# Kernel optimization log

Hardware: AMD Instinct MI355X
Metric: run time of the kernel (lower is better)

The kernel has to match this reference:

```python
import jax, jax.numpy as jnp
import numpy as np

STRIDE = 1

def setup_inputs() -> dict:
    key = jax.random.key(0)
    k1, k2 = jax.random.split(key)
    x = jax.random.normal(k1, (64, 16384), dtype=jnp.float32)        # (B, L)
    kernel = jax.random.normal(k2, (128, 16), dtype=jnp.float32) * 0.05  # (F, K) == phi
    return {"x": x, "kernel": kernel}

def reference(x, kernel):
    # Faithful math of SpecCnn1d_v01.call: the sparse phi places kernel[f, j]
    # at (f, i, i*stride + j), so phi @ x^T == windowed dot product.
    B, L = x.shape
    F, K = kernel.shape
    out_len = (L - K) // STRIDE + 1  # floor((L + 2*0 - K)/stride) + 1
    # Sliding windows: (out_len, K) gather indices -> windows (B, out_len, K)
    idx = jnp.arange(out_len)[:, None] * STRIDE + jnp.arange(K)[None, :]
    windows = x[:, idx]                       # (B, O, K)
    y = jnp.einsum('bok,fk->bof', windows, kernel)  # (B, O, F), matches perm [2,1,0]
    return jax.nn.relu(y)                     # activation='relu', use_bias=False
```

## Files before the change

### kernel.cpp

```cpp
#include <hip/hip_runtime.h>


constexpr int K_TAPS  = 16;
constexpr int F_FILT  = 128;
constexpr int O_TILE  = 64;
constexpr int O_CHUNK = 8;

__global__ __launch_bounds__(F_FILT) void SpecCnn1d_conv_kernel(
    const float* __restrict__ x,
    const float* __restrict__ w,
    float* __restrict__ y,
    int L, int out_len)
{
    const int f  = threadIdx.x;
    const int b  = blockIdx.y;
    const int o0 = blockIdx.x * O_TILE;

    float wr[K_TAPS];
    const float4* w4 = reinterpret_cast<const float4*>(w + f * K_TAPS);
    #pragma unroll
    for (int i = 0; i < K_TAPS / 4; ++i) {
        float4 v = w4[i];
        wr[4 * i + 0] = v.x;
        wr[4 * i + 1] = v.y;
        wr[4 * i + 2] = v.z;
        wr[4 * i + 3] = v.w;
    }

    const float* xb = x + (size_t)b * L;
    float*       yb = y + ((size_t)b * out_len + o0) * F_FILT + f;

    for (int oc = 0; oc < O_TILE; oc += O_CHUNK) {
        const int base = o0 + oc;

        float xs[O_CHUNK + K_TAPS - 1];
        #pragma unroll
        for (int j = 0; j < O_CHUNK + K_TAPS - 1; ++j) {
            int xi = base + j;
            xi = (xi < L) ? xi : (L - 1);
            xs[j] = xb[xi];
        }

        #pragma unroll
        for (int oo = 0; oo < O_CHUNK; ++oo) {
            float acc = 0.0f;
            #pragma unroll
            for (int k = 0; k < K_TAPS; ++k)
                acc = fmaf(xs[oo + k], wr[k], acc);
            const int o = base + oo;
            if (o < out_len)
                yb[(size_t)(oc + oo) * F_FILT] = fmaxf(acc, 0.0f);
        }
    }
}

extern "C" void kernel_launch(void* const* d_in, const int* in_sizes, int n_in,
                              void* d_out, int out_size, void* d_ws, size_t ws_size,
                              hipStream_t stream) {
    const float* x = (const float*)d_in[0];
    const float* w = (const float*)d_in[1];
    float*       y = (float*)d_out;

    const int B = 64;
    const int L = in_sizes[0] / B;
    const int out_len = L - K_TAPS + 1;

    dim3 grid((out_len + O_TILE - 1) / O_TILE, B);
    dim3 block(F_FILT);
    SpecCnn1d_conv_kernel<<<grid, block, 0, stream>>>(x, w, y, L, out_len);
}
```

Before: 543.2 us.

## Register-block four filters per thread with float4 loads and stores

```diff
diff --git a/kernel.cpp b/kernel.cpp
--- a/kernel.cpp
+++ b/kernel.cpp
@@ -4,52 +4,96 @@
 constexpr int K_TAPS  = 16;
 constexpr int F_FILT  = 128;
 constexpr int O_TILE  = 64;
-constexpr int O_CHUNK = 8;
+constexpr int O_PER_T = 8;
+constexpr int NTHREAD = 256;
 
-__global__ __launch_bounds__(F_FILT) void SpecCnn1d_conv_kernel(
+__global__ __launch_bounds__(NTHREAD) void SpecCnn1d_conv_kernel(
     const float* __restrict__ x,
     const float* __restrict__ w,
     float* __restrict__ y,
     int L, int out_len)
 {
-    const int f  = threadIdx.x;
+    const int f4 = threadIdx.x & 31;
+    const int g  = threadIdx.x >> 5;
     const int b  = blockIdx.y;
     const int o0 = blockIdx.x * O_TILE;
+    const int f  = f4 * 4;
 
-    float wr[K_TAPS];
-    const float4* w4 = reinterpret_cast<const float4*>(w + f * K_TAPS);
+    float wr[4][K_TAPS];
     #pragma unroll
-    for (int i = 0; i < K_TAPS / 4; ++i) {
-        float4 v = w4[i];
-        wr[4 * i + 0] = v.x;
-        wr[4 * i + 1] = v.y;
-        wr[4 * i + 2] = v.z;
-        wr[4 * i + 3] = v.w;
+    for (int ff = 0; ff < 4; ++ff) {
+        const float4* w4 = reinterpret_cast<const float4*>(w + (size_t)(f + ff) * K_TAPS);
+        #pragma unroll
+        for (int i = 0; i < K_TAPS / 4; ++i) {
+            float4 v = w4[i];
+            wr[ff][4 * i + 0] = v.x;
+            wr[ff][4 * i + 1] = v.y;
+            wr[ff][4 * i + 2] = v.z;
+            wr[ff][4 * i + 3] = v.w;
+        }
     }
 
     const float* xb = x + (size_t)b * L;
-    float*       yb = y + ((size_t)b * out_len + o0) * F_FILT + f;
+    const int    s  = o0 + g * O_PER_T;
+    float*       yb = y + ((size_t)b * out_len + s) * F_FILT + f;
 
-    for (int oc = 0; oc < O_TILE; oc += O_CHUNK) {
-        const int base = o0 + oc;
+    float xs[O_PER_T + K_TAPS];
 
-        float xs[O_CHUNK + K_TAPS - 1];
+    if (o0 + O_TILE + K_TAPS <= L) {
+        const float4* xv = reinterpret_cast<const float4*>(xb + s);
         #pragma unroll
-        for (int j = 0; j < O_CHUNK + K_TAPS - 1; ++j) {
-            int xi = base + j;
+        for (int i = 0; i < (O_PER_T + K_TAPS) / 4; ++i) {
+            float4 v = xv[i];
+            xs[4 * i + 0] = v.x;
+            xs[4 * i + 1] = v.y;
+            xs[4 * i + 2] = v.z;
+            xs[4 * i + 3] = v.w;
+        }
+
+        #pragma unroll
+        for (int oo = 0; oo < O_PER_T; ++oo) {
+            float a0 = 0.0f, a1 = 0.0f, a2 = 0.0f, a3 = 0.0f;
+            #pragma unroll
+            for (int k = 0; k < K_TAPS; ++k) {
+                const float xv_ = xs[oo + k];
+                a0 = fmaf(xv_, wr[0][k], a0);
+                a1 = fmaf(xv_, wr[1][k], a1);
+                a2 = fmaf(xv_, wr[2][k], a2);
+                a3 = fmaf(xv_, wr[3][k], a3);
+            }
+            float4 r;
+            r.x = fmaxf(a0, 0.0f);
+            r.y = fmaxf(a1, 0.0f);
+            r.z = fmaxf(a2, 0.0f);
+            r.w = fmaxf(a3, 0.0f);
+            *reinterpret_cast<float4*>(yb + (size_t)oo * F_FILT) = r;
+        }
+    } else {
+        #pragma unroll
+        for (int j = 0; j < O_PER_T + K_TAPS; ++j) {
+            int xi = s + j;
             xi = (xi < L) ? xi : (L - 1);
             xs[j] = xb[xi];
         }
 
         #pragma unroll
-        for (int oo = 0; oo < O_CHUNK; ++oo) {
-            float acc = 0.0f;
+        for (int oo = 0; oo < O_PER_T; ++oo) {
+            float a0 = 0.0f, a1 = 0.0f, a2 = 0.0f, a3 = 0.0f;
             #pragma unroll
-            for (int k = 0; k < K_TAPS; ++k)
-                acc = fmaf(xs[oo + k], wr[k], acc);
-            const int o = base + oo;
-            if (o < out_len)
-                yb[(size_t)(oc + oo) * F_FILT] = fmaxf(acc, 0.0f);
+            for (int k = 0; k < K_TAPS; ++k) {
+                const float xv_ = xs[oo + k];
+                a0 = fmaf(xv_, wr[0][k], a0);
+                a1 = fmaf(xv_, wr[1][k], a1);
+                a2 = fmaf(xv_, wr[2][k], a2);
+                a3 = fmaf(xv_, wr[3][k], a3);
+            }
+            float4 r;
+            r.x = fmaxf(a0, 0.0f);
+            r.y = fmaxf(a1, 0.0f);
+            r.z = fmaxf(a2, 0.0f);
+            r.w = fmaxf(a3, 0.0f);
+            if (s + oo < out_len)
+                *reinterpret_cast<float4*>(yb + (size_t)oo * F_FILT) = r;
         }
     }
 }
@@ -66,6 +110,6 @@
     const int out_len = L - K_TAPS + 1;
 
     dim3 grid((out_len + O_TILE - 1) / O_TILE, B);
-    dim3 block(F_FILT);
+    dim3 block(NTHREAD);
     SpecCnn1d_conv_kernel<<<grid, block, 0, stream>>>(x, w, y, L, out_len);
 }
```

After: 587.9 us. 1.08x slower.

## Compute two filters per thread with float2 stores and vectorized, double-buffered x loads

Applied to the files above, without the earlier changes.

```diff
diff --git a/kernel.cpp b/kernel.cpp
--- a/kernel.cpp
+++ b/kernel.cpp
@@ -5,51 +5,97 @@
 constexpr int F_FILT  = 128;
 constexpr int O_TILE  = 64;
 constexpr int O_CHUNK = 8;
+constexpr int NTHREAD = 64;
+constexpr int XS_N    = O_CHUNK + K_TAPS;
 
-__global__ __launch_bounds__(F_FILT) void SpecCnn1d_conv_kernel(
+__global__ __launch_bounds__(NTHREAD) void SpecCnn1d_conv_kernel(
     const float* __restrict__ x,
     const float* __restrict__ w,
     float* __restrict__ y,
     int L, int out_len)
 {
-    const int f  = threadIdx.x;
-    const int b  = blockIdx.y;
-    const int o0 = blockIdx.x * O_TILE;
+    const int lane = threadIdx.x;
+    const int f    = lane << 1;
+    const int b    = blockIdx.y;
+    const int o0   = blockIdx.x * O_TILE;
 
-    float wr[K_TAPS];
-    const float4* w4 = reinterpret_cast<const float4*>(w + f * K_TAPS);
-    #pragma unroll
-    for (int i = 0; i < K_TAPS / 4; ++i) {
-        float4 v = w4[i];
-        wr[4 * i + 0] = v.x;
-        wr[4 * i + 1] = v.y;
-        wr[4 * i + 2] = v.z;
-        wr[4 * i + 3] = v.w;
+    float w0[K_TAPS], w1[K_TAPS];
+    {
+        const float4* wp = reinterpret_cast<const float4*>(w + (size_t)f * K_TAPS);
+        #pragma unroll
+        for (int i = 0; i < K_TAPS / 4; ++i) {
+            float4 v0 = wp[i];
+            float4 v1 = wp[i + 4];
+            w0[4*i+0] = v0.x; w0[4*i+1] = v0.y; w0[4*i+2] = v0.z; w0[4*i+3] = v0.w;
+            w1[4*i+0] = v1.x; w1[4*i+1] = v1.y; w1[4*i+2] = v1.z; w1[4*i+3] = v1.w;
+        }
     }
 
     const float* xb = x + (size_t)b * L;
-    float*       yb = y + ((size_t)b * out_len + o0) * F_FILT + f;
+    float2* yb = reinterpret_cast<float2*>(y + ((size_t)b * out_len + o0) * F_FILT) + lane;
 
-    for (int oc = 0; oc < O_TILE; oc += O_CHUNK) {
-        const int base = o0 + oc;
+    if (o0 + O_TILE + K_TAPS <= L) {
+        float xs0[XS_N], xs1[XS_N];
 
-        float xs[O_CHUNK + K_TAPS - 1];
+        auto LOADU = [&](float* xs, int oc) {
+            const float4* xp = reinterpret_cast<const float4*>(xb + o0 + oc);
+            #pragma unroll
+            for (int i = 0; i < XS_N / 4; ++i) {
+                float4 v = xp[i];
+                xs[4*i+0] = v.x; xs[4*i+1] = v.y; xs[4*i+2] = v.z; xs[4*i+3] = v.w;
+            }
+        };
+        auto COMP = [&](const float* xs, int oc) {
+            #pragma unroll
+            for (int oo = 0; oo < O_CHUNK; ++oo) {
+                float a0 = 0.0f, a1 = 0.0f;
+                #pragma unroll
+                for (int k = 0; k < K_TAPS; ++k) {
+                    const float xv = xs[oo + k];
+                    a0 = fmaf(xv, w0[k], a0);
+                    a1 = fmaf(xv, w1[k], a1);
+                }
+                float2 r;
+                r.x = fmaxf(a0, 0.0f);
+                r.y = fmaxf(a1, 0.0f);
+                yb[(size_t)(oc + oo) * (F_FILT / 2)] = r;
+            }
+        };
+
+        LOADU(xs0, 0);
         #pragma unroll
-        for (int j = 0; j < O_CHUNK + K_TAPS - 1; ++j) {
-            int xi = base + j;
-            xi = (xi < L) ? xi : (L - 1);
-            xs[j] = xb[xi];
+        for (int oc = 0; oc < O_TILE; oc += 2 * O_CHUNK) {
+            LOADU(xs1, oc + O_CHUNK);
+            COMP(xs0, oc);
+            if (oc + 2 * O_CHUNK < O_TILE)
+                LOADU(xs0, oc + 2 * O_CHUNK);
+            COMP(xs1, oc + O_CHUNK);
         }
-
-        #pragma unroll
-        for (int oo = 0; oo < O_CHUNK; ++oo) {
-            float acc = 0.0f;
+    } else {
+        for (int oc = 0; oc < O_TILE; oc += O_CHUNK) {
+            const int base = o0 + oc;
+            float xs[XS_N];
             #pragma unroll
-            for (int k = 0; k < K_TAPS; ++k)
-                acc = fmaf(xs[oo + k], wr[k], acc);
-            const int o = base + oo;
-            if (o < out_len)
-                yb[(size_t)(oc + oo) * F_FILT] = fmaxf(acc, 0.0f);
+            for (int j = 0; j < XS_N; ++j) {
+                int xi = base + j;
+                xi = (xi < L) ? xi : (L - 1);
+                xs[j] = xb[xi];
+            }
+            #pragma unroll
+            for (int oo = 0; oo < O_CHUNK; ++oo) {
+                float a0 = 0.0f, a1 = 0.0f;
+                #pragma unroll
+                for (int k = 0; k < K_TAPS; ++k) {
+                    const float xv = xs[oo + k];
+                    a0 = fmaf(xv, w0[k], a0);
+                    a1 = fmaf(xv, w1[k], a1);
+                }
+                float2 r;
+                r.x = fmaxf(a0, 0.0f);
+                r.y = fmaxf(a1, 0.0f);
+                if (base + oo < out_len)
+                    yb[(size_t)(oc + oo) * (F_FILT / 2)] = r;
+            }
         }
     }
 }
@@ -66,6 +112,6 @@
     const int out_len = L - K_TAPS + 1;
 
     dim3 grid((out_len + O_TILE - 1) / O_TILE, B);
-    dim3 block(F_FILT);
+    dim3 block(NTHREAD);
     SpecCnn1d_conv_kernel<<<grid, block, 0, stream>>>(x, w, y, L, out_len);
 }
```

New measurement: 546.5 us. Within noise of the previous version (+0.6%).
